# Performance work log

Measured on AMD Instinct MI355X. Metric: run time of the kernel, lower is better.

The kernel has to match this reference:

```python
import jax, jax.numpy as jnp
import numpy as np

VOCAB = 10000
HID = 1024
OUT = 10000
BATCH = 32
SEQ = 256


def setup_inputs() -> dict:
    key = jax.random.key(0)
    k1, k2, k3, k4 = jax.random.split(key, 4)
    inputs = jax.random.randint(k1, (BATCH, SEQ), 0, VOCAB, dtype=jnp.int32)
    state = jnp.zeros((BATCH, HID), dtype=jnp.float32)
    W_xh = 0.01 * jax.random.normal(k2, (VOCAB, HID), dtype=jnp.float32)
    W_hh = 0.01 * jax.random.normal(k3, (HID, HID), dtype=jnp.float32)
    W_hq = 0.01 * jax.random.normal(k4, (HID, OUT), dtype=jnp.float32)
    b_h = jnp.zeros((HID,), dtype=jnp.float32)
    b_q = jnp.zeros((OUT,), dtype=jnp.float32)
    return {"inputs": inputs, "state": state, "W_xh": W_xh, "W_hh": W_hh,
            "b_h": b_h, "W_hq": W_hq, "b_q": b_q}


def reference(inputs, state, W_xh, W_hh, b_h, W_hq, b_q):
    # inputs: (B, T) int ids. Original one-hots then matmuls with W_xh;
    # one_hot(x) @ W_xh == W_xh[x], so we use the gather form (same math).
    x_tb = inputs.T  # (T, B)

    def step(H, x_t):
        # x_t: (B,) ids; H: (B, HID)
        H = jnp.tanh(W_xh[x_t] + H @ W_hh + b_h)
        Y = H @ W_hq + b_q  # (B, OUT)
        return H, Y

    H_final, Ys = jax.lax.scan(step, state, x_tb)  # Ys: (T, B, OUT)
    # torch.cat(outputs, dim=0) over the time list -> (T*B, OUT)
    Y = Ys.reshape(-1, Ys.shape[-1])
    return Y, H_final
```

## Files before the change

kernel.cpp:

```cpp
#include <hip/hip_runtime.h>
#include <hip/hip_bf16.h>

#define VOCAB 10000
#define HID   1024
#define OUTN  10000
#define BATCH 32
#define SEQT  256
#define NPAD  10112

typedef short s16x8 __attribute__((ext_vector_type(8)));
typedef float f32x4 __attribute__((ext_vector_type(4)));

#define GLOAD_LDS16(gptr, lptr)                                                      \
  __builtin_amdgcn_global_load_lds((__attribute__((address_space(1))) void*)(gptr),  \
                                   (__attribute__((address_space(3))) void*)(lptr),  \
                                   16, 0, 0)

__global__ __launch_bounds__(256) void transpose_cast(
    const float* __restrict__ src, __hip_bfloat16* __restrict__ dst,
    int K, int N, int Npad) {
  __shared__ float tile[32][33];
  const int n0 = blockIdx.x * 32, k0 = blockIdx.y * 32;
  const int tx = threadIdx.x & 31, ty = threadIdx.x >> 5;
#pragma unroll
  for (int yy = 0; yy < 32; yy += 8) {
    const int k = k0 + ty + yy, n = n0 + tx;
    tile[ty + yy][tx] = (k < K && n < N) ? src[k * N + n] : 0.f;
  }
  __syncthreads();
#pragma unroll
  for (int yy = 0; yy < 32; yy += 8) {
    const int n = n0 + ty + yy, k = k0 + tx;
    if (n < Npad && k < K) dst[(size_t)n * K + k] = __float2bfloat16(tile[tx][ty + yy]);
  }
}

__global__ __launch_bounds__(256) void cast_state(
    const float* __restrict__ s, __hip_bfloat16* __restrict__ d, int n,
    unsigned* __restrict__ counter) {
  const int i = blockIdx.x * 256 + threadIdx.x;
  if (i == 0) atomicExch(counter, 0u);
  if (i < n) d[i] = __float2bfloat16(s[i]);
}

__device__ __forceinline__ s16x8 load16_coherent(const void* p) {
  s16x8 v;
  asm volatile("global_load_dwordx4 %0, %1, off sc0 sc1"
               : "=v"(v) : "v"(p) : "memory");
  return v;
}
__device__ __forceinline__ void store2_coherent(void* p, unsigned short h) {
  unsigned u = h;
  asm volatile("global_store_short %0, %1, off sc0 sc1"
               :: "v"(p), "v"(u) : "memory");
}

__global__ __launch_bounds__(256, 1) void rnn_persist(
    __hip_bfloat16* __restrict__ Hbf,
    const int* __restrict__ ids,
    const float* __restrict__ W_xh,
    const __hip_bfloat16* __restrict__ WhhT,
    const float* __restrict__ b_h,
    float* __restrict__ Hfin,
    unsigned* __restrict__ counter) {
  const int wg   = blockIdx.x;
  const int wave = threadIdx.x >> 6;
  const int lane = threadIdx.x & 63;
  const int wm = wave >> 1, wn = wave & 1;
  const int row0 = wm * 16;
  const int col0 = wg * 32 + wn * 16;
  const int l16 = lane & 15;
  const int g   = lane >> 4;

  s16x8 breg[32];
  {
    const __hip_bfloat16* bBase = WhhT + (size_t)(col0 + l16) * HID + g * 8;
#pragma unroll
    for (int kk = 0; kk < 32; ++kk)
      breg[kk] = *reinterpret_cast<const s16x8*>(bBase + kk * 32);
  }

  const int ccol  = col0 + l16;
  const int crow0 = row0 + g * 4;
  const float bh = b_h[ccol];

  float wxh[4];
#pragma unroll
  for (int j = 0; j < 4; ++j)
    wxh[j] = W_xh[(size_t)ids[(crow0 + j) * SEQT + 0] * HID + ccol];

  const int aOff = (row0 + l16) * HID + g * 8;

  for (int t = 0; t < SEQT; ++t) {
    const __hip_bfloat16* aBase = Hbf + (size_t)t * BATCH * HID + aOff;
    __hip_bfloat16* Hnext = Hbf + (size_t)(t + 1) * BATCH * HID;

    s16x8 areg[32];
#pragma unroll
    for (int kk = 0; kk < 32; ++kk)
      areg[kk] = load16_coherent(aBase + kk * 32);
    asm volatile("s_waitcnt vmcnt(0)" ::: "memory");
    __builtin_amdgcn_sched_barrier(0);

    f32x4 acc0 = {0.f, 0.f, 0.f, 0.f}, acc1 = {0.f, 0.f, 0.f, 0.f};
#pragma unroll
    for (int kk = 0; kk < 32; kk += 2) {
      acc0 = __builtin_amdgcn_mfma_f32_16x16x32_bf16(areg[kk],     breg[kk],     acc0, 0, 0, 0);
      acc1 = __builtin_amdgcn_mfma_f32_16x16x32_bf16(areg[kk + 1], breg[kk + 1], acc1, 0, 0, 0);
    }

#pragma unroll
    for (int j = 0; j < 4; ++j) {
      const float x = acc0[j] + acc1[j] + wxh[j] + bh;
      const float e = __expf(2.f * x);
      const float v = 1.f - 2.f / (e + 1.f);
      const __hip_bfloat16 hv = __float2bfloat16(v);
      store2_coherent(Hnext + (crow0 + j) * HID + ccol,
                      *reinterpret_cast<const unsigned short*>(&hv));
      if (t == SEQT - 1) Hfin[(crow0 + j) * HID + ccol] = v;
    }

    if (t + 1 < SEQT) {
#pragma unroll
      for (int j = 0; j < 4; ++j)
        wxh[j] = W_xh[(size_t)ids[(crow0 + j) * SEQT + (t + 1)] * HID + ccol];
    }

    if (t + 1 < SEQT) {
      __syncthreads();
      if (threadIdx.x == 0) {
        atomicAdd(counter, 1u);
        const unsigned target = 32u * (unsigned)(t + 1);
        unsigned v;
        do {
          asm volatile("global_load_dword %0, %1, off sc0 sc1\n\t"
                       "s_waitcnt vmcnt(0)"
                       : "=v"(v) : "v"(counter) : "memory");
        } while (v < target);
      }
      __syncthreads();
    }
  }
}

__global__ __launch_bounds__(256) void gemm_out(
    const __hip_bfloat16* __restrict__ A,
    const __hip_bfloat16* __restrict__ BT,
    const float* __restrict__ b_q,
    float* __restrict__ Y) {
  __shared__ __align__(16) __hip_bfloat16 As[128 * 64];
  __shared__ __align__(16) __hip_bfloat16 Bs[128 * 64];

  const int bx = blockIdx.x;
  const int by = blockIdx.y;
  const int wave = threadIdx.x >> 6;
  const int lane = threadIdx.x & 63;
  const int wm = wave >> 1, wn = wave & 1;
  const int l16 = lane & 15;

  const size_t aRow0 = (size_t)by * 128;
  const size_t bRow0 = (size_t)bx * 128;

  f32x4 acc[4][4];
#pragma unroll
  for (int m = 0; m < 4; ++m)
#pragma unroll
    for (int n = 0; n < 4; ++n) acc[m][n] = (f32x4){0.f, 0.f, 0.f, 0.f};

  for (int kt = 0; kt < HID / 64; ++kt) {
    __syncthreads();
#pragma unroll
    for (int q = 0; q < 4; ++q) {
      const int ci = q * 256 + wave * 64 + lane;
      const int r  = ci >> 3;
      const int gc = (ci & 7) ^ (r & 7);
      const __hip_bfloat16* ga = A  + (aRow0 + r) * HID + kt * 64 + gc * 8;
      const __hip_bfloat16* gb = BT + (bRow0 + r) * HID + kt * 64 + gc * 8;
      GLOAD_LDS16(ga, &As[(q * 256 + wave * 64) * 8]);
      GLOAD_LDS16(gb, &Bs[(q * 256 + wave * 64) * 8]);
    }
    __syncthreads();

    s16x8 af[2][4], bf[2][4];
#pragma unroll
    for (int kc = 0; kc < 2; ++kc) {
      const int cc = kc * 4 + (lane >> 4);
#pragma unroll
      for (int m = 0; m < 4; ++m) {
        const int rowA = wm * 64 + m * 16 + l16;
        af[kc][m] = *reinterpret_cast<const s16x8*>(&As[rowA * 64 + ((cc ^ (rowA & 7)) * 8)]);
      }
#pragma unroll
      for (int n = 0; n < 4; ++n) {
        const int rowB = wn * 64 + n * 16 + l16;
        bf[kc][n] = *reinterpret_cast<const s16x8*>(&Bs[rowB * 64 + ((cc ^ (rowB & 7)) * 8)]);
      }
    }
#pragma unroll
    for (int kc = 0; kc < 2; ++kc)
#pragma unroll
      for (int m = 0; m < 4; ++m)
#pragma unroll
        for (int n = 0; n < 4; ++n)
          acc[m][n] = __builtin_amdgcn_mfma_f32_16x16x32_bf16(af[kc][m], bf[kc][n], acc[m][n], 0, 0, 0);
  }

  const int crow0 = by * 128 + wm * 64 + (lane >> 4) * 4;
  const int ccol0 = bx * 128 + wn * 64 + l16;
#pragma unroll
  for (int n = 0; n < 4; ++n) {
    const int ccol = ccol0 + n * 16;
    if (ccol < OUTN) {
      const float bq = b_q[ccol];
#pragma unroll
      for (int m = 0; m < 4; ++m) {
        const int crow = crow0 + m * 16;
#pragma unroll
        for (int j = 0; j < 4; ++j)
          Y[(size_t)(crow + j) * OUTN + ccol] = acc[m][n][j] + bq;
      }
    }
  }
}

extern "C" void kernel_launch(void* const* d_in, const int* in_sizes, int n_in,
                              void* d_out, int out_size, void* d_ws, size_t ws_size,
                              hipStream_t stream) {
  const int*   inputs = (const int*)d_in[0];
  const float* state  = (const float*)d_in[1];
  const float* W_xh   = (const float*)d_in[2];
  const float* W_hh   = (const float*)d_in[3];
  const float* b_h    = (const float*)d_in[4];
  const float* W_hq   = (const float*)d_in[5];
  const float* b_q    = (const float*)d_in[6];

  float* Y    = (float*)d_out;
  float* Hfin = Y + (size_t)SEQT * BATCH * OUTN;

  char* ws = (char*)d_ws;
  __hip_bfloat16* Hbf  = (__hip_bfloat16*)ws;
  __hip_bfloat16* WhhT = (__hip_bfloat16*)(ws + 16842752);
  __hip_bfloat16* WhqT = (__hip_bfloat16*)(ws + 16842752 + 2097152);
  unsigned* counter    = (unsigned*)(ws + 16842752 + 2097152 + 20709376 - 128);

  transpose_cast<<<dim3(32, 32), 256, 0, stream>>>(W_hh, WhhT, HID, HID, HID);
  transpose_cast<<<dim3(NPAD / 32, 32), 256, 0, stream>>>(W_hq, WhqT, HID, OUTN, NPAD);
  cast_state<<<dim3(BATCH * HID / 256), 256, 0, stream>>>(state, Hbf, BATCH * HID, counter);

  rnn_persist<<<dim3(32), dim3(256), 0, stream>>>(
      Hbf, inputs, W_xh, WhhT, b_h, Hfin, counter);

  gemm_out<<<dim3(NPAD / 128, 8192 / 128), 256, 0, stream>>>(Hbf + BATCH * HID, WhqT, b_q, Y);
}
```

Baseline: 1.937 ms.

## Stage W_hh slice in swizzled LDS and use immediate-offset coherent loads

The recurrent kernel now keeps its 32-column slice of transposed W_hh in a 64KB XOR-swizzled shared-memory buffer instead of 32 vector registers per lane. B fragments are read from LDS inside the MFMA loop. The H loads now use a single base register with immediate offsets. This frees a large block of VGPRs and cuts address arithmetic, in exchange for LDS reads on the serial critical path of each timestep. An explicit vmcnt wait before the barrier is also added so stores finish before the cross-block signal.

Result: slower. 2.003 ms (+3.5%).

```diff
diff --git a/kernel.cpp b/kernel.cpp
--- a/kernel.cpp
+++ b/kernel.cpp
@@ -16,6 +16,10 @@
                                    (__attribute__((address_space(3))) void*)(lptr),  \
                                    16, 0, 0)
 
+#define ALOAD16_SC(dst, base, off)                                                   \
+  asm volatile("global_load_dwordx4 %0, %1, off offset:%2 sc0 sc1"                   \
+               : "=v"(dst) : "v"(base), "n"(off) : "memory")
+
 __global__ __launch_bounds__(256) void transpose_cast(
     const float* __restrict__ src, __hip_bfloat16* __restrict__ dst,
     int K, int N, int Npad) {
@@ -41,18 +45,6 @@
   const int i = blockIdx.x * 256 + threadIdx.x;
   if (i == 0) atomicExch(counter, 0u);
   if (i < n) d[i] = __float2bfloat16(s[i]);
-}
-
-__device__ __forceinline__ s16x8 load16_coherent(const void* p) {
-  s16x8 v;
-  asm volatile("global_load_dwordx4 %0, %1, off sc0 sc1"
-               : "=v"(v) : "v"(p) : "memory");
-  return v;
-}
-__device__ __forceinline__ void store2_coherent(void* p, unsigned short h) {
-  unsigned u = h;
-  asm volatile("global_store_short %0, %1, off sc0 sc1"
-               :: "v"(p), "v"(u) : "memory");
 }
 
 __global__ __launch_bounds__(256, 1) void rnn_persist(
@@ -63,6 +55,8 @@
     const float* __restrict__ b_h,
     float* __restrict__ Hfin,
     unsigned* __restrict__ counter) {
+  __shared__ __align__(16) __hip_bfloat16 whh[32 * HID];
+
   const int wg   = blockIdx.x;
   const int wave = threadIdx.x >> 6;
   const int lane = threadIdx.x & 63;
@@ -72,12 +66,13 @@
   const int l16 = lane & 15;
   const int g   = lane >> 4;
 
-  s16x8 breg[32];
-  {
-    const __hip_bfloat16* bBase = WhhT + (size_t)(col0 + l16) * HID + g * 8;
-#pragma unroll
-    for (int kk = 0; kk < 32; ++kk)
-      breg[kk] = *reinterpret_cast<const s16x8*>(bBase + kk * 32);
+  for (int ci = threadIdx.x; ci < 32 * (HID / 8); ci += 256) {
+    const int col = ci >> 7;
+    const int c16 = ci & 127;
+    const s16x8 v = *reinterpret_cast<const s16x8*>(
+        WhhT + (size_t)(wg * 32 + col) * HID + c16 * 8);
+    const int sw = (c16 & ~7) | ((c16 & 7) ^ (col & 7));
+    *reinterpret_cast<s16x8*>(reinterpret_cast<char*>(whh) + col * 2048 + sw * 16) = v;
   }
 
   const int ccol  = col0 + l16;
@@ -89,24 +84,31 @@
   for (int j = 0; j < 4; ++j)
     wxh[j] = W_xh[(size_t)ids[(crow0 + j) * SEQT + 0] * HID + ccol];
 
+  __syncthreads();
+
   const int aOff = (row0 + l16) * HID + g * 8;
+  const char* myB = reinterpret_cast<const char*>(whh) + (wn * 16 + l16) * 2048;
+  const int xorv = l16 & 7;
+  const int offE = (g ^ xorv) * 16;
+  const int offO = ((g + 4) ^ xorv) * 16;
 
   for (int t = 0; t < SEQT; ++t) {
-    const __hip_bfloat16* aBase = Hbf + (size_t)t * BATCH * HID + aOff;
-    __hip_bfloat16* Hnext = Hbf + (size_t)(t + 1) * BATCH * HID;
+    const __hip_bfloat16* aBase = Hbf + (size_t)t * (BATCH * HID) + aOff;
+    __hip_bfloat16* Hnext = Hbf + (size_t)(t + 1) * (BATCH * HID);
 
     s16x8 areg[32];
 #pragma unroll
-    for (int kk = 0; kk < 32; ++kk)
-      areg[kk] = load16_coherent(aBase + kk * 32);
+    for (int kk = 0; kk < 32; ++kk) ALOAD16_SC(areg[kk], aBase, kk * 64);
     asm volatile("s_waitcnt vmcnt(0)" ::: "memory");
     __builtin_amdgcn_sched_barrier(0);
 
     f32x4 acc0 = {0.f, 0.f, 0.f, 0.f}, acc1 = {0.f, 0.f, 0.f, 0.f};
 #pragma unroll
     for (int kk = 0; kk < 32; kk += 2) {
-      acc0 = __builtin_amdgcn_mfma_f32_16x16x32_bf16(areg[kk],     breg[kk],     acc0, 0, 0, 0);
-      acc1 = __builtin_amdgcn_mfma_f32_16x16x32_bf16(areg[kk + 1], breg[kk + 1], acc1, 0, 0, 0);
+      const s16x8 b0 = *reinterpret_cast<const s16x8*>(myB + (kk >> 1) * 128 + offE);
+      const s16x8 b1 = *reinterpret_cast<const s16x8*>(myB + (kk >> 1) * 128 + offO);
+      acc0 = __builtin_amdgcn_mfma_f32_16x16x32_bf16(areg[kk],     b0, acc0, 0, 0, 0);
+      acc1 = __builtin_amdgcn_mfma_f32_16x16x32_bf16(areg[kk + 1], b1, acc1, 0, 0, 0);
     }
 
 #pragma unroll
@@ -115,8 +117,9 @@
       const float e = __expf(2.f * x);
       const float v = 1.f - 2.f / (e + 1.f);
       const __hip_bfloat16 hv = __float2bfloat16(v);
-      store2_coherent(Hnext + (crow0 + j) * HID + ccol,
-                      *reinterpret_cast<const unsigned short*>(&hv));
+      const unsigned u = *reinterpret_cast<const unsigned short*>(&hv);
+      asm volatile("global_store_short %0, %1, off sc0 sc1"
+                   :: "v"(Hnext + (crow0 + j) * HID + ccol), "v"(u) : "memory");
       if (t == SEQT - 1) Hfin[(crow0 + j) * HID + ccol] = v;
     }
 
@@ -127,6 +130,7 @@
     }
 
     if (t + 1 < SEQT) {
+      asm volatile("s_waitcnt vmcnt(0)" ::: "memory");
       __syncthreads();
       if (threadIdx.x == 0) {
         atomicAdd(counter, 1u);
```
